# Performance work log

Hardware: AMD Instinct MI355X
Metric: run time of the kernel (lower is better)

## Reference

```python
import jax, jax.numpy as jnp
import numpy as np

T, B, DIM, N = 2048, 16, 1024, 64
INIT_BETA_BIAS = 2.0
EPS = 1e-6


def setup_inputs() -> dict:
    key = jax.random.key(0)
    ks = jax.random.split(key, 6)
    xavier = np.sqrt(2.0 / (N + DIM)).astype(np.float32)
    return {
        "x": jax.random.normal(ks[0], (T, B, DIM), dtype=jnp.float32),
        "S0": jnp.zeros((B, N, N), dtype=jnp.float32),
        "W_k": jax.random.normal(ks[1], (N, DIM), dtype=jnp.float32) * xavier,
        "W_v": jax.random.normal(ks[2], (N, DIM), dtype=jnp.float32) * xavier,
        "W_q": jax.random.normal(ks[3], (N, DIM), dtype=jnp.float32) * xavier,
        "W_beta": jax.random.normal(ks[4], (N, DIM), dtype=jnp.float32) * xavier,
        "b_beta": jnp.full((N,), INIT_BETA_BIAS, dtype=jnp.float32),
    }


def reference(x, S0, W_k, W_v, W_q, W_beta, b_beta):
    # Batched projections: [T, B, dim] @ [dim, n] -> [T, B, n]
    k_all = jnp.einsum("tbd,nd->tbn", x, W_k)
    v_all = jnp.einsum("tbd,nd->tbn", x, W_v)
    q_all = jnp.einsum("tbd,nd->tbn", x, W_q)
    g_all = jax.nn.sigmoid(jnp.einsum("tbd,nd->tbn", x, W_beta) + b_beta)

    def step(S, inp):
        k, v, q, g = inp  # each [B, n]
        k_norm = k / (jnp.linalg.norm(k, axis=-1, keepdims=True) + EPS)
        retrieved = jnp.einsum("bij,bj->bi", S, k_norm)
        delta = v - retrieved
        S_new = g[:, :, None] * S + delta[:, :, None] * k_norm[:, None, :]
        Sq = jnp.einsum("bij,bj->bi", S_new, q)
        out = Sq * jax.nn.silu(Sq)  # self-gated output
        return S_new, out

    S_final, output = jax.lax.scan(step, S0, (k_all, v_all, q_all, g_all))
    return output, S_final
```

## Files before the change

kernel.cpp:

```cpp
#include <hip/hip_runtime.h>
#include <math.h>

#define T_STEPS 2048
#define BATCH   16
#define DIM     1024
#define NSTATE  64
#define NFIELD  256
#define PROJ_TSTRIDE (BATCH * NFIELD)
static constexpr float EPS = 1e-6f;

#define AS1 __attribute__((address_space(1)))
#define AS3 __attribute__((address_space(3)))

typedef _Float16 f16x8 __attribute__((ext_vector_type(8)));
typedef _Float16 f16x4 __attribute__((ext_vector_type(4)));
typedef float    f32x4 __attribute__((ext_vector_type(4)));

template <int CTRL>
__device__ __forceinline__ float dpp_add(float x) {
    int yi = __builtin_amdgcn_update_dpp(0, __float_as_int(x), CTRL, 0xF, 0xF, true);
    return x + __int_as_float(yi);
}
__device__ __forceinline__ float reduce16(float x) {
    x = dpp_add<0x121>(x);
    x = dpp_add<0x122>(x);
    x = dpp_add<0x124>(x);
    x = dpp_add<0x128>(x);
    return x;
}
__device__ __forceinline__ void reduce16x2(float& x, float& y) {
    x = dpp_add<0x121>(x); y = dpp_add<0x121>(y);
    x = dpp_add<0x122>(x); y = dpp_add<0x122>(y);
    x = dpp_add<0x124>(x); y = dpp_add<0x124>(y);
    x = dpp_add<0x128>(x); y = dpp_add<0x128>(y);
}
__device__ __forceinline__ float dot4r(const float4& u, const float4& w) {
    float t0 = u.x * w.x; t0 = fmaf(u.y, w.y, t0);
    float t1 = u.z * w.z; t1 = fmaf(u.w, w.w, t1);
    return reduce16(t0 + t1);
}


#define PBM   128
#define KSTEP 64
#define NKS   (DIM / KSTEP)

__global__ __launch_bounds__(256) void prep_w16(
    const float* __restrict__ Wk, const float* __restrict__ Wv,
    const float* __restrict__ Wq, const float* __restrict__ Wb,
    _Float16* __restrict__ W16)
{
    const int flat = blockIdx.x * 256 + threadIdx.x;
    const int lane = flat & 63;
    const int st   = (flat >> 6) & 31;
    const int ks   = flat >> 11;
    const int cg = st & 15, kc2 = st >> 4;
    const int col = cg * 16 + (lane & 15);
    const int field = col >> 6, wrow = col & 63;
    const float* Wf = (field == 0 ? Wk : field == 1 ? Wv : field == 2 ? Wq : Wb);
    const float* src = Wf + (size_t)wrow * DIM + ks * 64 + kc2 * 32 + (lane >> 4) * 8;
    const float4 a = *(const float4*)(src);
    const float4 b = *(const float4*)(src + 4);
    f16x8 r;
    r[0] = (_Float16)a.x; r[1] = (_Float16)a.y; r[2] = (_Float16)a.z; r[3] = (_Float16)a.w;
    r[4] = (_Float16)b.x; r[5] = (_Float16)b.y; r[6] = (_Float16)b.z; r[7] = (_Float16)b.w;
    *(f16x8*)(W16 + (size_t)flat * 8) = r;
}

__global__ __launch_bounds__(512) void proj_mfma(
    const float* __restrict__ x, const _Float16* __restrict__ W16,
    const float* __restrict__ bb, float* __restrict__ proj)
{
    __shared__ _Float16 Asub[2][16][64][8];
    __shared__ _Float16 Bsub[2][32][64][8];

    const int tid = threadIdx.x;
    const int w = tid >> 6, wl = tid & 63;
    const int wm = w >> 2, wn = w & 3;
    const int l15 = wl & 15, lr = wl >> 4;
    const size_t mbase = (size_t)blockIdx.x * PBM;

    _Float16* const abase = &Asub[0][0][0][0];
    _Float16* const bbase = &Bsub[0][0][0][0];

    const float* asrc[4];
    int aoff[4];
    #pragma unroll
    for (int it = 0; it < 4; ++it) {
        const int fid = it * 512 + tid;
        const int row = fid >> 4, kq = (fid & 15) * 4;
        asrc[it] = x + (mbase + row) * (size_t)DIM + kq;
        aoff[it] = ((kq >> 5) * 8 + (row >> 4)) * 512
                 + ((row & 15) + ((kq >> 3) & 3) * 16) * 8
                 + (kq & 7);
    }
    const _Float16* bsrc[4];
    int boff[4];
    #pragma unroll
    for (int m = 0; m < 4; ++m) {
        const int st = w * 4 + m;
        bsrc[m] = W16 + ((size_t)st * 64 + wl) * 8;
        boff[m] = st * 512;
    }

    auto stageB = [&](int ks, int buf) {
        #pragma unroll
        for (int m = 0; m < 4; ++m) {
            const _Float16* g = bsrc[m] + (size_t)ks * 16384;
            void* lp = (char*)bbase + (size_t)(buf * 16384 + boff[m]) * 2;
            __builtin_amdgcn_global_load_lds((const AS1 void*)g, (AS3 void*)lp, 16, 0, 0);
        }
    };

    float4 h0[4], h1[4];
    auto loadA = [&](int ks, float4* h) {
        #pragma unroll
        for (int it = 0; it < 4; ++it)
            h[it] = *(const float4*)(asrc[it] + ks * KSTEP);
    };
    auto writeA = [&](const float4* h, int buf) {
        #pragma unroll
        for (int it = 0; it < 4; ++it) {
            f16x4 v;
            v[0] = (_Float16)h[it].x; v[1] = (_Float16)h[it].y;
            v[2] = (_Float16)h[it].z; v[3] = (_Float16)h[it].w;
            *(f16x4*)(abase + buf * 8192 + aoff[it]) = v;
        }
    };

    f32x4 acc[4][4] = {};

    loadA(0, h0);
    stageB(0, 0);
    loadA(1, h1);
    writeA(h0, 0);
    __syncthreads();

    #pragma unroll
    for (int ks = 0; ks < NKS; ++ks) {
        const int buf = ks & 1;
        if (ks + 1 < NKS) stageB(ks + 1, buf ^ 1);
        if (ks + 2 < NKS) loadA(ks + 2, (ks & 1) ? h1 : h0);

        #pragma unroll
        for (int kc = 0; kc < 2; ++kc) {
            f16x8 af[4], bf[4];
            #pragma unroll
            for (int mf = 0; mf < 4; ++mf)
                af[mf] = *(const f16x8*)&Asub[buf][kc * 8 + wm * 4 + mf][wl][0];
            #pragma unroll
            for (int nf = 0; nf < 4; ++nf)
                bf[nf] = *(const f16x8*)&Bsub[buf][kc * 16 + wn * 4 + nf][wl][0];
            #pragma unroll
            for (int mf = 0; mf < 4; ++mf)
                #pragma unroll
                for (int nf = 0; nf < 4; ++nf)
                    acc[mf][nf] = __builtin_amdgcn_mfma_f32_16x16x32_f16(
                        af[mf], bf[nf], acc[mf][nf], 0, 0, 0);
        }

        if (ks + 1 < NKS) writeA((ks & 1) ? h0 : h1, buf ^ 1);
        __syncthreads();
    }

    if (wn == 0) {
        #pragma unroll
        for (int mf = 0; mf < 4; ++mf) {
            f32x4 s = acc[mf][0] * acc[mf][0];
            #pragma unroll
            for (int nf = 1; nf < 4; ++nf) s += acc[mf][nf] * acc[mf][nf];
            #pragma unroll
            for (int r = 0; r < 4; ++r) {
                float t = s[r];
                t += __shfl_xor(t, 1); t += __shfl_xor(t, 2);
                t += __shfl_xor(t, 4); t += __shfl_xor(t, 8);
                const float sc = 1.f / (sqrtf(t) + EPS);
                #pragma unroll
                for (int nf = 0; nf < 4; ++nf) acc[mf][nf][r] *= sc;
            }
        }
    }
    if (wn == 3) {
        #pragma unroll
        for (int nf = 0; nf < 4; ++nf) {
            const float bv = bb[nf * 16 + l15];
            #pragma unroll
            for (int mf = 0; mf < 4; ++mf)
                #pragma unroll
                for (int r = 0; r < 4; ++r)
                    acc[mf][nf][r] = 1.f / (1.f + __expf(-(acc[mf][nf][r] + bv)));
        }
    }

    #pragma unroll
    for (int mf = 0; mf < 4; ++mf)
        #pragma unroll
        for (int r = 0; r < 4; ++r) {
            float* dst = proj + (mbase + wm * 64 + mf * 16 + lr * 4 + r) * NFIELD
                              + wn * 64 + l15;
            dst[0]  = acc[mf][0][r];
            dst[16] = acc[mf][1][r];
            dst[32] = acc[mf][2][r];
            dst[48] = acc[mf][3][r];
        }
}

#define KAP_T 2112

__global__ __launch_bounds__(256) void kappa_kernel(
    const float* __restrict__ proj, float* __restrict__ kap2)
{
    const int tid = threadIdx.x;
    const int gid = blockIdx.x * 16 + (tid >> 4);
    const int l   = tid & 15;
    const int t = gid >> 4, b = gid & 15;
    if (t >= T_STEPS) {
        if (l == 0) *(float2*)(kap2 + (size_t)gid * 2) = make_float2(0.f, 0.f);
        return;
    }
    const float* base = proj + ((size_t)t * BATCH + b) * NFIELD;
    const float4 k0 = *(const float4*)(base + 4 * l);
    const float4 q0 = *(const float4*)(base + 128 + 4 * l);
    float cp = 0.f;
    float cq = 0.f;
    {
        float t0 = k0.x * q0.x; t0 = fmaf(k0.y, q0.y, t0);
        float t1 = k0.z * q0.z; t1 = fmaf(k0.w, q0.w, t1);
        cq = t0 + t1;
    }
    if (t + 1 < T_STEPS) {
        const float4 k1 = *(const float4*)(base + PROJ_TSTRIDE + 4 * l);
        float t0 = k0.x * k1.x; t0 = fmaf(k0.y, k1.y, t0);
        float t1 = k0.z * k1.z; t1 = fmaf(k0.w, k1.w, t1);
        cp = t0 + t1;
    }
    reduce16x2(cp, cq);
    if (l == 0) *(float2*)(kap2 + (size_t)gid * 2) = make_float2(cp, cq);
}


#define CH 32
#define NCHUNK (T_STEPS / CH)

__global__ __launch_bounds__(128) void scan_kernel(
    const float* __restrict__ proj,
    const float* __restrict__ kap2,
    const float* __restrict__ S0,
    float* __restrict__ out,
    float* __restrict__ Sfin)
{
    __shared__ float KQ[2][CH][128];
    __shared__ float VG[2][CH][16];
    __shared__ float KP2[2][CH][2];

    const int tid = threadIdx.x;
    const int l   = tid & 15;
    const int grp = tid >> 4;
    const int b   = blockIdx.x >> 3;
    const int i0  = (blockIdx.x & 7) * 8;
    const int i   = i0 + grp;
    const int c0  = l * 4;

    const size_t srow = ((size_t)(b * 64 + i)) * 64 + c0;
    float4 S = *(const float4*)(S0 + srow);

    const float* pb = proj + (size_t)b * NFIELD;
    const int wid = tid >> 6, wl = tid & 63;

    const int l31  = wl & 31;
    const int kq_f = l31 * 4 + ((l31 >= 16) ? 64 : 0);
    const int kq_s = wl >> 5;
    const int idx  = wl & 15;
    const int vg_f = (idx & 1) ? (192 + i0 + (idx >> 1)) : (64 + i0 + (idx >> 1));
    const int vg_s = wl >> 4;

    auto stage = [&](int c, int nb) {
        const float* cbase = pb + (size_t)c * CH * PROJ_TSTRIDE;
        #pragma unroll
        for (int m = 0; m < 8; ++m) {
            const int n = wid * 8 + m;
            const float* g = cbase + (size_t)(2 * n + kq_s) * PROJ_TSTRIDE + kq_f;
            void* lp = (char*)&KQ[nb][0][0] + n * 1024;
            __builtin_amdgcn_global_load_lds((const AS1 void*)g, (AS3 void*)lp, 16, 0, 0);
        }
        #pragma unroll
        for (int m = 0; m < 4; ++m) {
            const int p = wid * 4 + m;
            const float* g = cbase + (size_t)(4 * p + vg_s) * PROJ_TSTRIDE + vg_f;
            void* lp = (char*)&VG[nb][0][0] + p * 256;
            __builtin_amdgcn_global_load_lds((const AS1 void*)g, (AS3 void*)lp, 4, 0, 0);
        }
        if (wid == 0) {
            const float* g = kap2 + ((size_t)(c * CH + (wl >> 1)) * BATCH + b) * 2
                           + (wl & 1);
            void* lp = (char*)&KP2[nb][0][0];
            __builtin_amdgcn_global_load_lds((const AS1 void*)g, (AS3 void*)lp, 4, 0, 0);
        }
    };

    float4 kn_s[4], q_s[4];
    float2 vg_s4[4];
    auto ldslot = [&](int cb, int s, int j) {
        kn_s[j]  = *(const float4*)(&KQ[cb][s][c0]);
        q_s[j]   = *(const float4*)(&KQ[cb][s][64 + c0]);
        vg_s4[j] = *(const float2*)(&VG[cb][s][2 * grp]);
    };

    stage(0, 0);
    __syncthreads();

    float a;
    auto prime = [&](int nb) {
        #pragma unroll
        for (int j = 0; j < 4; ++j) ldslot(nb, j, j);
        a = dot4r(S, kn_s[0]);
    };
    prime(0);

    float osel = 0.f;

    for (int c = 0; c < NCHUNK; ++c) {
        const int cb = c & 1;
        const bool more = (c + 1 < NCHUNK);
        if (more) stage(c + 1, cb ^ 1);

        #pragma unroll
        for (int s = 0; s < CH; ++s) {
            const int j = s & 3;

            const float4 kn = kn_s[j], q = q_s[j];
            const float  v = vg_s4[j].x, g = vg_s4[j].y;
            const float4 knn = kn_s[(s + 1) & 3];
            const float2 kk = *(const float2*)&KP2[cb][s][0];

            if (s + 4 < CH) ldslot(cb, s + 4, j);

            float cq;
            {
                float t0 = S.x * q.x; t0 = fmaf(S.y, q.y, t0);
                float t1 = S.z * q.z; t1 = fmaf(S.w, q.w, t1);
                cq = t0 + t1;
            }
            float cp = 0.f;
            if (s + 1 < CH) {
                float t0 = S.x * knn.x; t0 = fmaf(S.y, knn.y, t0);
                float t1 = S.z * knn.z; t1 = fmaf(S.w, knn.w, t1);
                cp = t0 + t1;
            }
            reduce16x2(cp, cq);

            const float d = v - a;
            S.x = fmaf(d, kn.x, g * S.x);
            S.y = fmaf(d, kn.y, g * S.y);
            S.z = fmaf(d, kn.z, g * S.z);
            S.w = fmaf(d, kn.w, g * S.w);

            const float sq = fmaf(d, kk.y, g * cq);
            if (s + 1 < CH) a = fmaf(d, kk.x, g * cp);

            osel = ((s & 15) == l) ? sq : osel;
            if ((s & 15) == 15) {
                const float y = osel * osel / (1.f + __expf(-osel));
                const int tbase = c * CH + (s - 15);
                out[((size_t)(tbase + l) * BATCH + b) * 64 + i] = y;
            }
        }

        if (more) {
            __syncthreads();
            prime(cb ^ 1);
        }
    }

    *(float4*)(Sfin + srow) = S;
}

extern "C" void kernel_launch(void* const* d_in, const int* in_sizes, int n_in,
                              void* d_out, int out_size, void* d_ws, size_t ws_size,
                              hipStream_t stream) {
    const float* x  = (const float*)d_in[0];
    const float* S0 = (const float*)d_in[1];
    const float* Wk = (const float*)d_in[2];
    const float* Wv = (const float*)d_in[3];
    const float* Wq = (const float*)d_in[4];
    const float* Wb = (const float*)d_in[5];
    const float* bb = (const float*)d_in[6];

    float* out  = (float*)d_out;
    float* Sfin = out + (size_t)T_STEPS * BATCH * NSTATE;

    float*    proj = (float*)d_ws;
    float*    kap2 = proj + (size_t)T_STEPS * BATCH * NFIELD;
    _Float16* W16  = (_Float16*)(kap2 + (size_t)KAP_T * BATCH * 2);

    prep_w16<<<128, 256, 0, stream>>>(Wk, Wv, Wq, Wb, W16);
    proj_mfma<<<(T_STEPS * BATCH) / PBM, 512, 0, stream>>>(x, W16, bb, proj);
    kappa_kernel<<<KAP_T, 256, 0, stream>>>(proj, kap2);
    scan_kernel<<<(BATCH * NSTATE) / 8, 128, 0, stream>>>(proj, kap2, S0, out, Sfin);
}
```

Baseline: 422.6 us.

## Software-pipeline scan reductions one step ahead and prefetch kappa into registers

```diff
diff --git a/kernel.cpp b/kernel.cpp
--- a/kernel.cpp
+++ b/kernel.cpp
@@ -34,10 +34,13 @@
     x = dpp_add<0x124>(x); y = dpp_add<0x124>(y);
     x = dpp_add<0x128>(x); y = dpp_add<0x128>(y);
 }
-__device__ __forceinline__ float dot4r(const float4& u, const float4& w) {
+__device__ __forceinline__ float dotp(const float4& u, const float4& w) {
     float t0 = u.x * w.x; t0 = fmaf(u.y, w.y, t0);
     float t1 = u.z * w.z; t1 = fmaf(u.w, w.w, t1);
-    return reduce16(t0 + t1);
+    return t0 + t1;
+}
+__device__ __forceinline__ float dot4r(const float4& u, const float4& w) {
+    return reduce16(dotp(u, w));
 }
 
 
@@ -67,7 +70,7 @@
     *(f16x8*)(W16 + (size_t)flat * 8) = r;
 }
 
-__global__ __launch_bounds__(512) void proj_mfma(
+__global__ __launch_bounds__(512, 1) void proj_mfma(
     const float* __restrict__ x, const _Float16* __restrict__ W16,
     const float* __restrict__ bb, float* __restrict__ proj)
 {
@@ -222,17 +225,10 @@
     const float4 k0 = *(const float4*)(base + 4 * l);
     const float4 q0 = *(const float4*)(base + 128 + 4 * l);
     float cp = 0.f;
-    float cq = 0.f;
-    {
-        float t0 = k0.x * q0.x; t0 = fmaf(k0.y, q0.y, t0);
-        float t1 = k0.z * q0.z; t1 = fmaf(k0.w, q0.w, t1);
-        cq = t0 + t1;
-    }
+    float cq = dotp(k0, q0);
     if (t + 1 < T_STEPS) {
         const float4 k1 = *(const float4*)(base + PROJ_TSTRIDE + 4 * l);
-        float t0 = k0.x * k1.x; t0 = fmaf(k0.y, k1.y, t0);
-        float t1 = k0.z * k1.z; t1 = fmaf(k0.w, k1.w, t1);
-        cp = t0 + t1;
+        cp = dotp(k0, k1);
     }
     reduce16x2(cp, cq);
     if (l == 0) *(float2*)(kap2 + (size_t)gid * 2) = make_float2(cp, cq);
@@ -242,7 +238,7 @@
 #define CH 32
 #define NCHUNK (T_STEPS / CH)
 
-__global__ __launch_bounds__(128) void scan_kernel(
+__global__ __launch_bounds__(128, 1) void scan_kernel(
     const float* __restrict__ proj,
     const float* __restrict__ kap2,
     const float* __restrict__ S0,
@@ -299,21 +295,27 @@
     };
 
     float4 kn_s[4], q_s[4];
-    float2 vg_s4[4];
-    auto ldslot = [&](int cb, int s, int j) {
-        kn_s[j]  = *(const float4*)(&KQ[cb][s][c0]);
-        q_s[j]   = *(const float4*)(&KQ[cb][s][64 + c0]);
-        vg_s4[j] = *(const float2*)(&VG[cb][s][2 * grp]);
+    float2 vg_s4[4], kk_s[4];
+    auto ldslot = [&](int cb2, int s, int j) {
+        kn_s[j]  = *(const float4*)(&KQ[cb2][s][c0]);
+        q_s[j]   = *(const float4*)(&KQ[cb2][s][64 + c0]);
+        vg_s4[j] = *(const float2*)(&VG[cb2][s][2 * grp]);
+        kk_s[j]  = *(const float2*)(&KP2[cb2][s][0]);
     };
 
     stage(0, 0);
     __syncthreads();
 
-    float a;
+    float a, cqr, cpr;
     auto prime = [&](int nb) {
         #pragma unroll
         for (int j = 0; j < 4; ++j) ldslot(nb, j, j);
-        a = dot4r(S, kn_s[0]);
+        float aP  = dotp(S, kn_s[0]);
+        float cqP = dotp(S, q_s[0]);
+        float cpP = dotp(S, kn_s[1]);
+        reduce16x2(aP, cqP);
+        cpP = reduce16(cpP);
+        a = aP; cqr = cqP; cpr = cpP;
     };
     prime(0);
 
@@ -328,35 +330,30 @@
         for (int s = 0; s < CH; ++s) {
             const int j = s & 3;
 
-            const float4 kn = kn_s[j], q = q_s[j];
+            const float4 kn = kn_s[j];
             const float  v = vg_s4[j].x, g = vg_s4[j].y;
-            const float4 knn = kn_s[(s + 1) & 3];
-            const float2 kk = *(const float2*)&KP2[cb][s][0];
-
-            if (s + 4 < CH) ldslot(cb, s + 4, j);
-
-            float cq;
-            {
-                float t0 = S.x * q.x; t0 = fmaf(S.y, q.y, t0);
-                float t1 = S.z * q.z; t1 = fmaf(S.w, q.w, t1);
-                cq = t0 + t1;
-            }
-            float cp = 0.f;
-            if (s + 1 < CH) {
-                float t0 = S.x * knn.x; t0 = fmaf(S.y, knn.y, t0);
-                float t1 = S.z * knn.z; t1 = fmaf(S.w, knn.w, t1);
-                cp = t0 + t1;
-            }
-            reduce16x2(cp, cq);
-
-            const float d = v - a;
+            const float2 kk = kk_s[j];
+
+            const float d  = v - a;
+            const float sq = fmaf(d, kk.y, g * cqr);
+            const float an = fmaf(d, kk.x, g * cpr);
+
             S.x = fmaf(d, kn.x, g * S.x);
             S.y = fmaf(d, kn.y, g * S.y);
             S.z = fmaf(d, kn.z, g * S.z);
             S.w = fmaf(d, kn.w, g * S.w);
 
-            const float sq = fmaf(d, kk.y, g * cq);
-            if (s + 1 < CH) a = fmaf(d, kk.x, g * cp);
+            if (s + 4 < CH) ldslot(cb, s + 4, j);
+
+            if (s + 2 < CH) {
+                float cqP = dotp(S, q_s[(s + 1) & 3]);
+                float cpP = dotp(S, kn_s[(s + 2) & 3]);
+                reduce16x2(cpP, cqP);
+                cpr = cpP; cqr = cqP;
+            } else if (s + 1 < CH) {
+                cqr = reduce16(dotp(S, q_s[(s + 1) & 3]));
+            }
+            a = an;
 
             osel = ((s & 15) == l) ? sq : osel;
             if ((s & 15) == 15) {
```

After: 416.3 us. Within noise of the previous version (-1.5%).
